# Performance work log

Hardware: AMD Instinct MI355X
Metric: run time of the kernel (lower is better)

The kernel has to match this reference:

```python
import jax, jax.numpy as jnp
import numpy as np


def setup_inputs() -> dict:
    key = jax.random.key(0)
    k1, k2 = jax.random.split(key)
    N, C = 8, 3
    H, W = 256, 256          # kernel-prediction grid
    KSIZE = 5                # kernels channel dim = 4 * KSIZE**2 = 100
    feat_in = jax.random.normal(k1, (N, C, 2 * H, 2 * W), dtype=jnp.float32)
    kernel = jax.random.normal(k2, (N, 4 * KSIZE * KSIZE, H, W), dtype=jnp.float32)
    return {"feat_in": feat_in, "kernel": kernel, "ksize": KSIZE}


def reference(feat_in, kernel, ksize):
    """Faithful JAX port of the customized FAC (filter-adaptive convolution).

    feat_in: (N, 3, 2H, 2W)  high-res features
    kernel : (N, 4*ksize^2, H, W)  per-pixel predicted filter taps
    output : (N, 3, H, W)
    """
    N, C, H2, W2 = feat_in.shape
    _, kch, H, W = kernel.shape
    pad = (ksize - 1) // 2

    # F.pad(..., mode='replicate')
    fp = jnp.pad(feat_in, ((0, 0), (0, 0), (pad, pad), (pad, pad)), mode='edge')

    # torch unfold(2, ksize, 1).unfold(3, ksize, 1) -> (N, C, H2, W2, kh, kw)
    patches = jnp.stack(
        [jnp.stack([fp[:, :, i:i + H2, j:j + W2] for j in range(ksize)], axis=-1)
         for i in range(ksize)], axis=-2)

    # permute(0,2,3,1,5,4) -> (N, H2, W2, C, kw, kh); contiguous reshape
    # reinterprets the (2H, 2W, C, k, k) block as (H, W, C, 4k^2)
    x = jnp.transpose(patches, (0, 2, 3, 1, 5, 4))
    x = x.reshape(N, H, W, C, ksize * ksize * 4)

    # kernel path (channels == 3, kernels == 4k^2 branch)
    k = jnp.transpose(kernel, (0, 2, 3, 1)).reshape(N, H, W, 1, 2 * ksize, 2 * ksize)
    k = jnp.concatenate([k, k, k], axis=3)              # broadcast to 3 channels
    k = jnp.transpose(k, (0, 1, 2, 3, 5, 4)).reshape(N, H, W, C, -1)

    out = jnp.sum(x * k, axis=-1)                       # (N, H, W, C)
    return jnp.transpose(out, (0, 3, 1, 2))             # (N, C, H, W)
```

## Files before the change

kernel.cpp:

```cpp
#include <hip/hip_runtime.h>


#define HH 256
#define WW 256
#define H2 512
#define W2 512
#define KPLANE (HH * WW)
#define KP4 (KPLANE / 4)

typedef float f32x4_t __attribute__((ext_vector_type(4)));

__global__ __launch_bounds__(256, 2) void fac_fused4(const float* __restrict__ feat,
                                                     const float* __restrict__ kern,
                                                     float* __restrict__ out) {
    int t  = blockIdx.x * 256 + threadIdx.x;
    int qp = t & 63;
    int h  = (t >> 6) & 255;
    int n  = t >> 14;
    int w  = qp << 2;

    int hi = (qp >> 5) & 1;
    int xb = (qp & 31) << 4;
    int y2 = 2 * h + hi;

    bool e0 = (qp & 31) == 0;
    bool e1 = (qp & 31) == 31;
    int wbase = e0 ? 0 : (e1 ? 488 : (xb - 4));

    const f32x4_t* kp4 = (const f32x4_t*)(kern + (size_t)n * 100 * KPLANE +
                                          (size_t)h * WW + w);

    const int d_tab[4][3] = {{0,1,2},{0,1,3},{0,2,3},{1,2,3}};
    const int c_tab[4][3] = {{0,1,2},{1,2,0},{2,0,1},{0,1,2}};

    float acc[3][4] = {};

#pragma unroll 1
    for (int i = 0; i < 5; ++i) {
        int sy = min(max(y2 + i - 2, 0), H2 - 1);

        float fr[3][20];
#pragma unroll
        for (int c = 0; c < 3; ++c) {
            const float* rp = feat + ((size_t)(n * 3 + c) * H2 + sy) * W2 + wbase;
            float4 q0 = *(const float4*)(rp);
            float4 q1 = *(const float4*)(rp + 4);
            float4 q2 = *(const float4*)(rp + 8);
            float4 q3 = *(const float4*)(rp + 12);
            float4 q4 = *(const float4*)(rp + 16);
            float4 q5 = *(const float4*)(rp + 20);
            float win[24] = {q0.x, q0.y, q0.z, q0.w, q1.x, q1.y, q1.z, q1.w,
                             q2.x, q2.y, q2.z, q2.w, q3.x, q3.y, q3.z, q3.w,
                             q4.x, q4.y, q4.z, q4.w, q5.x, q5.y, q5.z, q5.w};
#pragma unroll
            for (int o = 0; o < 20; ++o) {
                const int i_in = o + 2;
                const int i_e0 = (o - 2) < 0 ? 0 : (o - 2);
                const int i_e1 = (o + 6) > 23 ? 23 : (o + 6);
                fr[c][o] = e0 ? win[i_e0] : (e1 ? win[i_e1] : win[i_in]);
            }
        }

        const f32x4_t* kpi = kp4 + (size_t)i * 10 * KP4;
#pragma unroll
        for (int tb = 0; tb < 4; ++tb) {
#pragma unroll
            for (int j = 0; j < 5; ++j) {
                const int a5 = 5 * tb + j;
                const int kc = (a5 & 1) * 50 + (a5 >> 1);
                f32x4_t kv = *(kpi + (size_t)kc * KP4);

                const int d0 = d_tab[tb][0], c0 = c_tab[tb][0];
                const int d1 = d_tab[tb][1], c1 = c_tab[tb][1];
                const int d2 = d_tab[tb][2], c2 = c_tab[tb][2];
#pragma unroll
                for (int p = 0; p < 4; ++p) {
                    acc[0][p] += kv[p] * fr[c0][d0 + j + 4 * p];
                    acc[1][p] += kv[p] * fr[c1][d1 + j + 4 * p];
                    acc[2][p] += kv[p] * fr[c2][d2 + j + 4 * p];
                }
            }
        }
    }

    float* op = out + (size_t)n * 3 * KPLANE + (size_t)h * WW + w;
#pragma unroll
    for (int c = 0; c < 3; ++c) {
        *(float4*)(op + (size_t)c * KPLANE) =
            make_float4(acc[c][0], acc[c][1], acc[c][2], acc[c][3]);
    }
}

extern "C" void kernel_launch(void* const* d_in, const int* in_sizes, int n_in,
                              void* d_out, int out_size, void* d_ws, size_t ws_size,
                              hipStream_t stream) {
    const float* feat = (const float*)d_in[0];
    const float* kern = (const float*)d_in[1];
    float* out = (float*)d_out;

    fac_fused4<<<512, 256, 0, stream>>>(feat, kern, out);
}
```

Baseline: 52.46 us.

## Software-pipeline kernel tap loads across rows with nontemporal loads

Splits each row's 20 kernel-tap vector loads into two halves and prefetches the first half of the next row while the current row's FMAs run. This double buffering is meant to hide global-memory latency, since only 2 waves per SIMD are resident. The loads also switch to nontemporal hints because the kernel tensor is streamed once. The extra 30 live float4 registers per thread raise register pressure and may cause spills under the launch bound of 256 threads and 2 blocks.

```diff
diff --git a/kernel.cpp b/kernel.cpp
--- a/kernel.cpp
+++ b/kernel.cpp
@@ -10,9 +10,46 @@
 
 typedef float f32x4_t __attribute__((ext_vector_type(4)));
 
-__global__ __launch_bounds__(256, 2) void fac_fused4(const float* __restrict__ feat,
-                                                     const float* __restrict__ kern,
-                                                     float* __restrict__ out) {
+template <int TB0>
+__device__ __forceinline__ void load10(const f32x4_t* __restrict__ kpi,
+                                       f32x4_t (&kv)[10]) {
+#pragma unroll
+    for (int tt = 0; tt < 2; ++tt)
+#pragma unroll
+        for (int j = 0; j < 5; ++j) {
+            const int a5 = 5 * (TB0 + tt) + j;
+            const int kc = (a5 & 1) * 50 + (a5 >> 1);
+            kv[tt * 5 + j] = __builtin_nontemporal_load(kpi + (size_t)kc * KP4);
+        }
+}
+
+template <int TB0>
+__device__ __forceinline__ void fma10(const f32x4_t (&kv)[10],
+                                      const float (&fr)[3][20], float (&acc)[3][4]) {
+    constexpr int d_tab[4][3] = {{0,1,2},{0,1,3},{0,2,3},{1,2,3}};
+    constexpr int c_tab[4][3] = {{0,1,2},{1,2,0},{2,0,1},{0,1,2}};
+#pragma unroll
+    for (int tt = 0; tt < 2; ++tt) {
+        const int tb = TB0 + tt;
+        const int d0 = d_tab[tb][0], c0 = c_tab[tb][0];
+        const int d1 = d_tab[tb][1], c1 = c_tab[tb][1];
+        const int d2 = d_tab[tb][2], c2 = c_tab[tb][2];
+#pragma unroll
+        for (int j = 0; j < 5; ++j) {
+            f32x4_t kv4 = kv[tt * 5 + j];
+#pragma unroll
+            for (int p = 0; p < 4; ++p) {
+                acc[0][p] += kv4[p] * fr[c0][d0 + j + 4 * p];
+                acc[1][p] += kv4[p] * fr[c1][d1 + j + 4 * p];
+                acc[2][p] += kv4[p] * fr[c2][d2 + j + 4 * p];
+            }
+        }
+    }
+}
+
+__global__ __launch_bounds__(256, 2) void fac_fused4p(const float* __restrict__ feat,
+                                                      const float* __restrict__ kern,
+                                                      float* __restrict__ out) {
     int t  = blockIdx.x * 256 + threadIdx.x;
     int qp = t & 63;
     int h  = (t >> 6) & 255;
@@ -30,10 +67,10 @@
     const f32x4_t* kp4 = (const f32x4_t*)(kern + (size_t)n * 100 * KPLANE +
                                           (size_t)h * WW + w);
 
-    const int d_tab[4][3] = {{0,1,2},{0,1,3},{0,2,3},{1,2,3}};
-    const int c_tab[4][3] = {{0,1,2},{1,2,0},{2,0,1},{0,1,2}};
+    float acc[3][4] = {};
+    f32x4_t kvA[10], kvB[10], kvN[10] = {};
 
-    float acc[3][4] = {};
+    load10<0>(kp4, kvA);
 
 #pragma unroll 1
     for (int i = 0; i < 5; ++i) {
@@ -62,25 +99,14 @@
         }
 
         const f32x4_t* kpi = kp4 + (size_t)i * 10 * KP4;
+        load10<2>(kpi, kvB);
+        if (i < 4) load10<0>(kpi + 10 * KP4, kvN);
+
+        fma10<0>(kvA, fr, acc);
+        fma10<2>(kvB, fr, acc);
+
 #pragma unroll
-        for (int tb = 0; tb < 4; ++tb) {
-#pragma unroll
-            for (int j = 0; j < 5; ++j) {
-                const int a5 = 5 * tb + j;
-                const int kc = (a5 & 1) * 50 + (a5 >> 1);
-                f32x4_t kv = *(kpi + (size_t)kc * KP4);
-
-                const int d0 = d_tab[tb][0], c0 = c_tab[tb][0];
-                const int d1 = d_tab[tb][1], c1 = c_tab[tb][1];
-                const int d2 = d_tab[tb][2], c2 = c_tab[tb][2];
-#pragma unroll
-                for (int p = 0; p < 4; ++p) {
-                    acc[0][p] += kv[p] * fr[c0][d0 + j + 4 * p];
-                    acc[1][p] += kv[p] * fr[c1][d1 + j + 4 * p];
-                    acc[2][p] += kv[p] * fr[c2][d2 + j + 4 * p];
-                }
-            }
-        }
+        for (int u = 0; u < 10; ++u) kvA[u] = kvN[u];
     }
 
     float* op = out + (size_t)n * 3 * KPLANE + (size_t)h * WW + w;
@@ -98,5 +124,5 @@
     const float* kern = (const float*)d_in[1];
     float* out = (float*)d_out;
 
-    fac_fused4<<<512, 256, 0, stream>>>(feat, kern, out);
+    fac_fused4p<<<512, 256, 0, stream>>>(feat, kern, out);
 }
```

New measurement: 45.06 us. 1.16x faster.
